# Performance work log

Measured on AMD Instinct MI355X. Metric: run time of the kernel, lower is better.

## Reference

```python
import jax, jax.numpy as jnp
import numpy as np

FP8_MAX = 448.0          # E4M3 max representable
SAFETY_MARGIN = 1.1
SCALE_CAP = 10000.0


def _fp8_scale(t):
    """Per-tensor dynamic scale (single step: tracked amax == current amax)."""
    amax = jax.lax.stop_gradient(jnp.max(jnp.abs(t)))
    scale = FP8_MAX / (amax * SAFETY_MARGIN)
    scale = jnp.where(amax == 0.0, 1.0, jnp.minimum(scale, SCALE_CAP))
    return scale


def _quantize_e4m3(t, scale):
    """Scale, clamp to E4M3 range, round to fp8, return dequantized-to-fp32 codes."""
    ts = jnp.clip(t * scale, -FP8_MAX, FP8_MAX)
    return ts.astype(jnp.float8_e4m3fn).astype(jnp.float32)


def setup_inputs() -> dict:
    key = jax.random.key(0)
    k1, k2, k3 = jax.random.split(key, 3)
    B, S, D_IN, D_OUT = 4, 2048, 4096, 4096
    x = jax.random.normal(k1, (B, S, D_IN), dtype=jnp.float32)
    weight = jax.random.normal(k2, (D_OUT, D_IN), dtype=jnp.float32) * 0.02
    bias = jax.random.normal(k3, (D_OUT,), dtype=jnp.float32) * 0.02
    return {"x": x, "weight": weight, "bias": bias}


def reference(x, weight, bias):
    orig_shape = x.shape
    x2 = x.reshape(-1, orig_shape[-1])               # [M, d_in]

    x_scale = _fp8_scale(x2)
    w_scale = _fp8_scale(weight)

    x_fp8 = _quantize_e4m3(x2, x_scale)              # fp8 codes held in fp32
    w_fp8 = _quantize_e4m3(weight, w_scale)

    # torch._scaled_mm: out = (x_fp8 @ w_fp8^T) * scale_a * scale_b, scale_* = 1/scale
    out = jnp.einsum('mk,nk->mn', x_fp8, w_fp8) * (1.0 / x_scale) * (1.0 / w_scale)
    out = out.reshape(*orig_shape[:-1], out.shape[-1])
    out = out + bias
    return out
```

## Files before the change

### kernel.cpp

```cpp
#include <hip/hip_runtime.h>
#include <hip/hip_bf16.h>

typedef float f32x16 __attribute__((ext_vector_type(16)));
typedef int   i32x8  __attribute__((ext_vector_type(8)));
typedef int   i32x4  __attribute__((ext_vector_type(4)));

#define FP8_MAX 448.0f


__device__ __forceinline__ void g2l16(const void* g, void* l) {
    __builtin_amdgcn_global_load_lds(
        (const __attribute__((address_space(1))) void*)g,
        (__attribute__((address_space(3))) void*)l,
        16, 0, 0);
}

__device__ __forceinline__ float scale_from(float amax) {
    float s = FP8_MAX / (amax * 1.1f);
    return (amax == 0.0f) ? 1.0f : fminf(s, 10000.0f);
}


__global__ void init_kernel(unsigned* amax) {
    amax[0] = 0u;
    amax[1] = 0u;
}

__global__ void amax_fused_kernel(const float* __restrict__ x, size_t nx,
                                  const float* __restrict__ w, size_t nw,
                                  unsigned* __restrict__ amax, int xblocks) {
    const float* src;
    size_t n;
    unsigned* out;
    int bid, nb;
    if ((int)blockIdx.x < xblocks) {
        src = x; n = nx; out = amax; bid = blockIdx.x; nb = xblocks;
    } else {
        src = w; n = nw; out = amax + 1; bid = blockIdx.x - xblocks; nb = gridDim.x - xblocks;
    }
    float m = 0.0f;
    const size_t ustep = (size_t)blockDim.x * 4;
    const size_t chunkf = ustep * 8;
    size_t base = (size_t)bid * chunkf + (size_t)threadIdx.x * 4;
    const size_t gstride = (size_t)nb * chunkf;
    for (; base < n; base += gstride) {
        float4 v[8];
        #pragma unroll
        for (int u = 0; u < 8; ++u) {
            size_t idx = base + (size_t)u * ustep;
            float4 vv = {0.0f, 0.0f, 0.0f, 0.0f};
            if (idx < n) vv = *(const float4*)(src + idx);
            v[u] = vv;
        }
        #pragma unroll
        for (int u = 0; u < 8; ++u)
            m = fmaxf(m, fmaxf(fmaxf(fabsf(v[u].x), fabsf(v[u].y)),
                               fmaxf(fabsf(v[u].z), fabsf(v[u].w))));
    }
    #pragma unroll
    for (int off = 32; off > 0; off >>= 1)
        m = fmaxf(m, __shfl_xor(m, off));
    __shared__ float sm[4];
    if ((threadIdx.x & 63) == 0) sm[threadIdx.x >> 6] = m;
    __syncthreads();
    if (threadIdx.x == 0) {
        float mm = fmaxf(fmaxf(sm[0], sm[1]), fmaxf(sm[2], sm[3]));
        atomicMax(out, __float_as_uint(mm));
    }
}

__device__ __forceinline__ float qclamp(float v, float s) {
    return fminf(fmaxf(v * s, -FP8_MAX), FP8_MAX);
}

__global__ void quant_fused_kernel(const float* __restrict__ x, size_t nx,
                                   const float* __restrict__ w, size_t nw,
                                   const unsigned* __restrict__ amax,
                                   unsigned char* __restrict__ xq,
                                   unsigned char* __restrict__ wq, int xblocks) {
    const float* src;
    size_t n;
    unsigned char* dst;
    int bid, nb, sel;
    if ((int)blockIdx.x < xblocks) {
        src = x; n = nx; dst = xq; bid = blockIdx.x; nb = xblocks; sel = 0;
    } else {
        src = w; n = nw; dst = wq; bid = blockIdx.x - xblocks; nb = gridDim.x - xblocks; sel = 1;
    }
    const float s = scale_from(__uint_as_float(amax[sel]));
    const size_t ustep = (size_t)blockDim.x * 4;
    const size_t chunkf = ustep * 4;
    size_t base = (size_t)bid * chunkf + (size_t)threadIdx.x * 4;
    const size_t gstride = (size_t)nb * chunkf;
    for (; base < n; base += gstride) {
        float4 v[4];
        bool ok[4];
        #pragma unroll
        for (int u = 0; u < 4; ++u) {
            size_t idx = base + (size_t)u * ustep;
            ok[u] = idx < n;
            float4 vv = {0.0f, 0.0f, 0.0f, 0.0f};
            if (ok[u]) vv = *(const float4*)(src + idx);
            v[u] = vv;
        }
        #pragma unroll
        for (int u = 0; u < 4; ++u) {
            if (ok[u]) {
                int p = __builtin_amdgcn_cvt_pk_fp8_f32(qclamp(v[u].x, s), qclamp(v[u].y, s), 0, false);
                p = __builtin_amdgcn_cvt_pk_fp8_f32(qclamp(v[u].z, s), qclamp(v[u].w, s), p, true);
                *(unsigned*)(dst + base + (size_t)u * ustep) = (unsigned)p;
            }
        }
    }
}

#define BM 128
#define BN 256
#define BKB 64

__global__ __launch_bounds__(256, 2) void gemm_fp8_kernel(
    const unsigned char* __restrict__ Aq,
    const unsigned char* __restrict__ Bq,
    const float* __restrict__ bias,
    const unsigned* __restrict__ amax,
    float* __restrict__ out,
    int M, int N, int K) {
    __shared__ alignas(16) unsigned char sA[3][BM * BKB];
    __shared__ alignas(16) unsigned char sB[3][BN * BKB];

    const int tid = threadIdx.x;
    const int wave = tid >> 6;
    const int lane = tid & 63;
    const int r31 = lane & 31;
    const int half = lane >> 5;

    int nwg = (int)gridDim.x;
    int bid = (int)blockIdx.x;
    if ((nwg & 7) == 0) {
        int cpx = nwg >> 3;
        bid = (bid & 7) * cpx + (bid >> 3);
    }
    const int nbn = N / BN;
    const int brow = (bid / nbn) * BM;
    const int bcol = (bid % nbn) * BN;

    const int wr = (wave >> 1) * 64;
    const int wc = (wave & 1) * 128;

    f32x16 acc[2][4] = {};

    const int NT = K / BKB;
    const int j0 = tid * 16;

    auto stageA = [&](int slot, int t) {
        #pragma unroll
        for (int j = 0; j < 2; ++j) {
            int oo = j * 4096 + j0;
            int r = oo >> 6;
            int c = (oo & 63) ^ (((r >> 1) & 3) << 4);
            g2l16(Aq + (size_t)(brow + r) * K + t * BKB + c,
                  &sA[slot][j * 4096 + wave * 1024]);
        }
    };
    auto stageB = [&](int slot, int t) {
        #pragma unroll
        for (int j = 0; j < 4; ++j) {
            int oo = j * 4096 + j0;
            int r = oo >> 6;
            int c = (oo & 63) ^ (((r >> 1) & 3) << 4);
            g2l16(Bq + (size_t)(bcol + r) * K + t * BKB + c,
                  &sB[slot][j * 4096 + wave * 1024]);
        }
    };
    auto rdA = [&](int slot, int row) -> i32x8 {
        const unsigned char* base = &sA[slot][row * BKB];
        int swz = ((row >> 1) & 3) << 4;
        int kb = half * 32;
        union { i32x8 v8; i32x4 v4[2]; } u;
        u.v4[0] = *(const i32x4*)(base + (kb ^ swz));
        u.v4[1] = *(const i32x4*)(base + ((kb + 16) ^ swz));
        return u.v8;
    };
    auto rdB = [&](int slot, int row) -> i32x8 {
        const unsigned char* base = &sB[slot][row * BKB];
        int swz = ((row >> 1) & 3) << 4;
        int kb = half * 32;
        union { i32x8 v8; i32x4 v4[2]; } u;
        u.v4[0] = *(const i32x4*)(base + (kb ^ swz));
        u.v4[1] = *(const i32x4*)(base + ((kb + 16) ^ swz));
        return u.v8;
    };

    #define MM(a, b, c) \
        c = __builtin_amdgcn_mfma_scale_f32_32x32x64_f8f6f4( \
            a, b, c, 0, 0, 0, 0x7f7f7f7f, 0, 0x7f7f7f7f)

    stageA(0, 0); stageB(0, 0);
    stageA(1, 1); stageB(1, 1);

    int sr = 0;
    for (int t = 0; t < NT; ++t) {
        int tt = t + 2;
        if (tt >= NT) tt -= NT;
        int ss = sr + 2; if (ss >= 3) ss -= 3;
        stageA(ss, tt);
        stageB(ss, tt);
        asm volatile("s_waitcnt vmcnt(6)" ::: "memory");
        __builtin_amdgcn_s_barrier();

        i32x8 a[2], b[4];
        #pragma unroll
        for (int m = 0; m < 2; ++m) a[m] = rdA(sr, wr + m * 32 + r31);
        #pragma unroll
        for (int n = 0; n < 4; ++n) b[n] = rdB(sr, wc + n * 32 + r31);
        #pragma unroll
        for (int m = 0; m < 2; ++m)
            #pragma unroll
            for (int n = 0; n < 4; ++n)
                MM(a[m], b[n], acc[m][n]);
        __builtin_amdgcn_s_barrier();

        sr = sr + 1; if (sr >= 3) sr = 0;
    }

    const float invx = 1.0f / scale_from(__uint_as_float(amax[0]));
    const float invw = 1.0f / scale_from(__uint_as_float(amax[1]));
    const float s2 = invx * invw;
    #pragma unroll
    for (int n = 0; n < 4; ++n) {
        int col = bcol + wc + n * 32 + r31;
        float bv = bias[col];
        #pragma unroll
        for (int m = 0; m < 2; ++m) {
            int rbase = brow + wr + m * 32 + half * 4;
            #pragma unroll
            for (int r = 0; r < 16; ++r) {
                int row = rbase + (r & 3) + 8 * (r >> 2);
                out[(size_t)row * N + col] = acc[m][n][r] * s2 + bv;
            }
        }
    }
    #undef MM
}


extern "C" void kernel_launch(void* const* d_in, const int* in_sizes, int n_in,
                              void* d_out, int out_size, void* d_ws, size_t ws_size,
                              hipStream_t stream) {
    const float* x    = (const float*)d_in[0];
    const float* w    = (const float*)d_in[1];
    const float* bias = (const float*)d_in[2];
    float* out = (float*)d_out;

    const size_t nx = (size_t)in_sizes[0];
    const size_t nw = (size_t)in_sizes[1];
    const int N = in_sizes[2];
    const int K = (int)(nw / (size_t)N);
    const int M = (int)(nx / (size_t)K);

    unsigned* amax = (unsigned*)d_ws;
    unsigned char* xq = (unsigned char*)d_ws + 256;
    unsigned char* wq = xq + nx;

    const int TOTB = 2048;
    int xb = (int)((double)TOTB * (double)nx / (double)(nx + nw));
    if (xb < 1) xb = 1;
    if (xb > TOTB - 1) xb = TOTB - 1;

    init_kernel<<<1, 1, 0, stream>>>(amax);
    amax_fused_kernel<<<TOTB, 256, 0, stream>>>(x, nx, w, nw, amax, xb);
    quant_fused_kernel<<<TOTB, 256, 0, stream>>>(x, nx, w, nw, amax, xq, wq, xb);

    dim3 grid((M / BM) * (N / BN));
    gemm_fp8_kernel<<<grid, 256, 0, stream>>>(xq, wq, bias, amax, out, M, N, K);
}
```

Baseline: 247.0 us.

## Load GEMM fragments directly from global memory into registers, dropping LDS staging

Removes the triple-buffered LDS staging with global_load_lds and barriers. Each lane now loads its MFMA operand fragments straight from global memory into registers, double-buffered with vmcnt waits and raised wave priority around the MFMA block. This avoids the LDS round trip and the workgroup barriers. In exchange, waves no longer share tile data, so global and L2 traffic rises because each wave re-fetches its own A and B rows. The per-lane row-strided 16-byte loads are also poorly coalesced.

```diff
diff --git a/kernel.cpp b/kernel.cpp
--- a/kernel.cpp
+++ b/kernel.cpp
@@ -7,13 +7,6 @@
 
 #define FP8_MAX 448.0f
 
-
-__device__ __forceinline__ void g2l16(const void* g, void* l) {
-    __builtin_amdgcn_global_load_lds(
-        (const __attribute__((address_space(1))) void*)g,
-        (__attribute__((address_space(3))) void*)l,
-        16, 0, 0);
-}
 
 __device__ __forceinline__ float scale_from(float amax) {
     float s = FP8_MAX / (amax * 1.1f);
@@ -125,9 +118,6 @@
     const unsigned* __restrict__ amax,
     float* __restrict__ out,
     int M, int N, int K) {
-    __shared__ alignas(16) unsigned char sA[3][BM * BKB];
-    __shared__ alignas(16) unsigned char sB[3][BN * BKB];
-
     const int tid = threadIdx.x;
     const int wave = tid >> 6;
     const int lane = tid & 63;
@@ -150,77 +140,67 @@
     f32x16 acc[2][4] = {};
 
     const int NT = K / BKB;
-    const int j0 = tid * 16;
-
-    auto stageA = [&](int slot, int t) {
-        #pragma unroll
-        for (int j = 0; j < 2; ++j) {
-            int oo = j * 4096 + j0;
-            int r = oo >> 6;
-            int c = (oo & 63) ^ (((r >> 1) & 3) << 4);
-            g2l16(Aq + (size_t)(brow + r) * K + t * BKB + c,
-                  &sA[slot][j * 4096 + wave * 1024]);
-        }
-    };
-    auto stageB = [&](int slot, int t) {
-        #pragma unroll
-        for (int j = 0; j < 4; ++j) {
-            int oo = j * 4096 + j0;
-            int r = oo >> 6;
-            int c = (oo & 63) ^ (((r >> 1) & 3) << 4);
-            g2l16(Bq + (size_t)(bcol + r) * K + t * BKB + c,
-                  &sB[slot][j * 4096 + wave * 1024]);
-        }
-    };
-    auto rdA = [&](int slot, int row) -> i32x8 {
-        const unsigned char* base = &sA[slot][row * BKB];
-        int swz = ((row >> 1) & 3) << 4;
-        int kb = half * 32;
-        union { i32x8 v8; i32x4 v4[2]; } u;
-        u.v4[0] = *(const i32x4*)(base + (kb ^ swz));
-        u.v4[1] = *(const i32x4*)(base + ((kb + 16) ^ swz));
-        return u.v8;
-    };
-    auto rdB = [&](int slot, int row) -> i32x8 {
-        const unsigned char* base = &sB[slot][row * BKB];
-        int swz = ((row >> 1) & 3) << 4;
-        int kb = half * 32;
-        union { i32x8 v8; i32x4 v4[2]; } u;
-        u.v4[0] = *(const i32x4*)(base + (kb ^ swz));
-        u.v4[1] = *(const i32x4*)(base + ((kb + 16) ^ swz));
-        return u.v8;
-    };
-
+
+    const size_t sK = (size_t)K;
+    size_t ao[2], bo[4];
+    #pragma unroll
+    for (int m = 0; m < 2; ++m)
+        ao[m] = (size_t)(brow + wr + m * 32 + r31) * sK + half * 32;
+    #pragma unroll
+    for (int n = 0; n < 4; ++n)
+        bo[n] = (size_t)(bcol + wc + n * 32 + r31) * sK + half * 32;
+
+    #define LD8(P) ({ union { i32x8 v8; i32x4 v4[2]; } _u;                      \
+                      _u.v4[0] = *(const i32x4*)(P);                            \
+                      _u.v4[1] = *(const i32x4*)((P) + 16);                     \
+                      _u.v8; })
     #define MM(a, b, c) \
         c = __builtin_amdgcn_mfma_scale_f32_32x32x64_f8f6f4( \
             a, b, c, 0, 0, 0, 0x7f7f7f7f, 0, 0x7f7f7f7f)
 
-    stageA(0, 0); stageB(0, 0);
-    stageA(1, 1); stageB(1, 1);
-
-    int sr = 0;
-    for (int t = 0; t < NT; ++t) {
-        int tt = t + 2;
-        if (tt >= NT) tt -= NT;
-        int ss = sr + 2; if (ss >= 3) ss -= 3;
-        stageA(ss, tt);
-        stageB(ss, tt);
-        asm volatile("s_waitcnt vmcnt(6)" ::: "memory");
-        __builtin_amdgcn_s_barrier();
-
-        i32x8 a[2], b[4];
-        #pragma unroll
-        for (int m = 0; m < 2; ++m) a[m] = rdA(sr, wr + m * 32 + r31);
-        #pragma unroll
-        for (int n = 0; n < 4; ++n) b[n] = rdB(sr, wc + n * 32 + r31);
+    i32x8 aX[2], bX[4], aY[2], bY[4];
+
+    #pragma unroll
+    for (int m = 0; m < 2; ++m) aX[m] = LD8(Aq + ao[m]);
+    #pragma unroll
+    for (int n = 0; n < 4; ++n) bX[n] = LD8(Bq + bo[n]);
+
+    for (int t = 0; t < NT; t += 2) {
+        {
+            const size_t off = (size_t)(t + 1) * BKB;
+            #pragma unroll
+            for (int m = 0; m < 2; ++m) aY[m] = LD8(Aq + ao[m] + off);
+            #pragma unroll
+            for (int n = 0; n < 4; ++n) bY[n] = LD8(Bq + bo[n] + off);
+        }
+        asm volatile("s_waitcnt vmcnt(12)" ::: "memory");
+        __builtin_amdgcn_sched_barrier(0);
+        __builtin_amdgcn_s_setprio(1);
         #pragma unroll
         for (int m = 0; m < 2; ++m)
             #pragma unroll
             for (int n = 0; n < 4; ++n)
-                MM(a[m], b[n], acc[m][n]);
-        __builtin_amdgcn_s_barrier();
-
-        sr = sr + 1; if (sr >= 3) sr = 0;
+                MM(aX[m], bX[n], acc[m][n]);
+        __builtin_amdgcn_s_setprio(0);
+        __builtin_amdgcn_sched_barrier(0);
+
+        {
+            const size_t off = (t + 2 < NT) ? (size_t)(t + 2) * BKB : 0;
+            #pragma unroll
+            for (int m = 0; m < 2; ++m) aX[m] = LD8(Aq + ao[m] + off);
+            #pragma unroll
+            for (int n = 0; n < 4; ++n) bX[n] = LD8(Bq + bo[n] + off);
+        }
+        asm volatile("s_waitcnt vmcnt(12)" ::: "memory");
+        __builtin_amdgcn_sched_barrier(0);
+        __builtin_amdgcn_s_setprio(1);
+        #pragma unroll
+        for (int m = 0; m < 2; ++m)
+            #pragma unroll
+            for (int n = 0; n < 4; ++n)
+                MM(aY[m], bY[n], acc[m][n]);
+        __builtin_amdgcn_s_setprio(0);
+        __builtin_amdgcn_sched_barrier(0);
     }
 
     const float invx = 1.0f / scale_from(__uint_as_float(amax[0]));
@@ -241,6 +221,7 @@
         }
     }
     #undef MM
+    #undef LD8
 }
 
 
```

Result: slower. 448.0 us (+81.4%).
